# Performance work log

Hardware: AMD Instinct MI355X
Metric: run time of the kernel (lower is better)

## Reference

```python
import jax, jax.numpy as jnp
import numpy as np

B, S = 128, 400
EMB, ENC, DEC = 128, 1024, 300
VOCAB, MAX_OOV = 50000, 50


def setup_inputs() -> dict:
    key = jax.random.key(0)
    ks = jax.random.split(key, 16)
    s = 0.05
    return {
        "embedded": jax.random.normal(ks[0], (B, EMB), jnp.float32),
        "enc_output": jax.random.normal(ks[1], (B, S, ENC), jnp.float32),
        "h1": jax.random.normal(ks[2], (B, DEC), jnp.float32),
        "pad_mask": jnp.zeros((B, S), jnp.bool_),
        "max_n_oov": MAX_OOV,
        "source_WORD_encoding_extended": jax.random.randint(ks[3], (B, S), 0, VOCAB + MAX_OOV),
        # parameters
        "W_attn1": jax.random.normal(ks[4], (ENC, DEC), jnp.float32) * s,
        "W_attn2": jax.random.normal(ks[5], (ENC, DEC), jnp.float32) * s,
        "W_ih": jax.random.normal(ks[6], (3 * DEC, EMB + ENC), jnp.float32) * s,
        "W_hh": jax.random.normal(ks[7], (3 * DEC, DEC), jnp.float32) * s,
        "b_ih": jax.random.normal(ks[8], (3 * DEC,), jnp.float32) * s,
        "b_hh": jax.random.normal(ks[9], (3 * DEC,), jnp.float32) * s,
        "W_out": jax.random.normal(ks[10], (VOCAB, ENC + DEC), jnp.float32) * s,
        "b_out": jax.random.normal(ks[11], (VOCAB,), jnp.float32) * s,
        "W_p": jax.random.normal(ks[12], (1, ENC + DEC), jnp.float32) * s,
        "b_p": jax.random.normal(ks[13], (1,), jnp.float32) * s,
    }


def _additive_attn(h, enc_output, W, pad_mask):
    # h: [B, DEC], enc_output: [B, S, ENC], W: [ENC, DEC]
    e = jnp.einsum('bse,ed->bsd', enc_output, W)
    scores = jnp.einsum('bd,bsd->bs', h, e)
    scores = jnp.where(pad_mask, -jnp.inf, scores)
    return jax.nn.softmax(scores, axis=1)  # [B, S]


def _gru_cell(x, h, W_ih, W_hh, b_ih, b_hh):
    gx = x @ W_ih.T + b_ih  # [B, 3*DEC]
    gh = h @ W_hh.T + b_hh
    xr, xz, xn = jnp.split(gx, 3, axis=1)
    hr, hz, hn = jnp.split(gh, 3, axis=1)
    r = jax.nn.sigmoid(xr + hr)
    z = jax.nn.sigmoid(xz + hz)
    n = jnp.tanh(xn + r * hn)
    return (1.0 - z) * n + z * h


def reference(embedded, enc_output, h1, pad_mask, max_n_oov,
              source_WORD_encoding_extended, W_attn1, W_attn2,
              W_ih, W_hh, b_ih, b_hh, W_out, b_out, W_p, b_p):
    a = _additive_attn(h1, enc_output, W_attn1, pad_mask)
    weighted = jnp.einsum('bs,bse->be', a, enc_output)
    rnn_input = jnp.concatenate([embedded, weighted], axis=1)
    h_new = _gru_cell(rnn_input, h1, W_ih, W_hh, b_ih, b_hh)

    a2 = _additive_attn(h_new, enc_output, W_attn2, pad_mask)
    weighted2 = jnp.einsum('bs,bse->be', a2, enc_output)
    hw = jnp.concatenate([h_new, weighted2], axis=1)  # [B, DEC+ENC]

    p_vocab = jax.nn.softmax(hw @ W_out.T + b_out, axis=1)  # [B, VOCAB]
    p_gen = jax.nn.sigmoid(hw @ W_p.T + b_p)  # [B, 1]

    bsz = p_vocab.shape[0]
    ext_zeros = jnp.zeros((bsz, max_n_oov), p_vocab.dtype)
    p_out = p_gen * jnp.concatenate([p_vocab, ext_zeros], axis=1)
    rows = jnp.arange(bsz)[:, None]
    p_out = p_out.at[rows, source_WORD_encoding_extended].add((1.0 - p_gen) * a2)
    return p_out, h_new
```

## Files before the change

### kernel.cpp

```cpp
#include <hip/hip_runtime.h>
#include <stdint.h>

constexpr int B_     = 128;
constexpr int S_     = 400;
constexpr int EMB_   = 128;
constexpr int ENC_   = 1024;
constexpr int DEC_   = 300;
constexpr int VOCAB_ = 50000;
constexpr int OOV_   = 50;
constexpr int OUTW_  = VOCAB_ + OOV_;
constexpr int KHW_   = ENC_ + DEC_;
constexpr int KHWP_  = 1344;
constexpr int G3_    = 3 * DEC_;
constexpr int KIN_   = EMB_ + ENC_;
constexpr int CHK_   = 64;
constexpr int CHKB_  = 128;
constexpr int NC_    = 21;
constexpr int PSTRIDE_ = 1028;
constexpr int NTILE_ = 782;
constexpr int NSPL_  = 6;
constexpr int ROWS_  = 67;
constexpr int NBLK_  = 768;

typedef __attribute__((ext_vector_type(4))) float f32x4;
typedef __attribute__((ext_vector_type(8))) short short8;

__device__ __forceinline__ float dot4(float4 a, float4 b) {
  return a.x * b.x + a.y * b.y + a.z * b.z + a.w * b.w;
}

__device__ __forceinline__ short f2bf(float f) {
  uint32_t u = __builtin_bit_cast(uint32_t, f);
  u += 0x7fffu + ((u >> 16) & 1u);
  return (short)(u >> 16);
}

__device__ __forceinline__ void gbar(int* bar, int target) {
  __syncthreads();
  if (threadIdx.x == 0) {
    __hip_atomic_fetch_add(bar, 1, __ATOMIC_RELEASE, __HIP_MEMORY_SCOPE_AGENT);
    while (__hip_atomic_load(bar, __ATOMIC_ACQUIRE, __HIP_MEMORY_SCOPE_AGENT) < target)
      __builtin_amdgcn_s_sleep(8);
  }
  __syncthreads();
}


__device__ void ph_compute_v(const float* __restrict__ W, const float* __restrict__ h,
                             float* __restrict__ v, int b, int tid, float* hs) {
  for (int d = tid; d < DEC_; d += 256) hs[d] = h[b * DEC_ + d];
  __syncthreads();
  for (int e = tid; e < ENC_; e += 256) {
    const float4* w4 = (const float4*)(W + (size_t)e * DEC_);
    const float4* h4 = (const float4*)hs;
    float acc = 0.f;
    #pragma unroll 5
    for (int d = 0; d < DEC_ / 4; ++d) acc += dot4(w4[d], h4[d]);
    v[b * ENC_ + e] = acc;
  }
  __syncthreads();
}

__device__ void ph_attn(const float* __restrict__ enc, const float* __restrict__ v,
                        float* __restrict__ scores, float* __restrict__ part,
                        int b, int split, int tid) {
  int wave = tid >> 6, lane = tid & 63;
  float4 vr[4];
  #pragma unroll
  for (int c = 0; c < 4; ++c) vr[c] = *(const float4*)(v + b * ENC_ + c * 256 + lane * 4);
  float m = -INFINITY, l = 0.f;
  float4 wa[4];
  #pragma unroll
  for (int c = 0; c < 4; ++c) wa[c] = make_float4(0.f, 0.f, 0.f, 0.f);
  int s0 = split * ROWS_;
  int s_end = min(s0 + ROWS_, S_);
  int s = s0 + wave;
  for (; s + 4 < s_end; s += 8) {
    const float* era = enc + ((size_t)b * S_ + s) * ENC_;
    const float* erb = enc + ((size_t)b * S_ + s + 4) * ENC_;
    float4 e4a[4], e4b[4];
    #pragma unroll
    for (int c = 0; c < 4; ++c) {
      e4a[c] = *(const float4*)(era + c * 256 + lane * 4);
      e4b[c] = *(const float4*)(erb + c * 256 + lane * 4);
    }
    float pa = 0.f, pb = 0.f;
    #pragma unroll
    for (int c = 0; c < 4; ++c) { pa += dot4(e4a[c], vr[c]); pb += dot4(e4b[c], vr[c]); }
    #pragma unroll
    for (int off = 32; off; off >>= 1) {
      pa += __shfl_xor(pa, off);
      pb += __shfl_xor(pb, off);
    }
    if (lane == 0) { scores[b * S_ + s] = pa; scores[b * S_ + s + 4] = pb; }
    float nm = fmaxf(m, fmaxf(pa, pb));
    float sc = __expf(m - nm);
    float ea = __expf(pa - nm);
    float eb = __expf(pb - nm);
    l = l * sc + ea + eb;
    #pragma unroll
    for (int c = 0; c < 4; ++c) {
      wa[c].x = wa[c].x * sc + ea * e4a[c].x + eb * e4b[c].x;
      wa[c].y = wa[c].y * sc + ea * e4a[c].y + eb * e4b[c].y;
      wa[c].z = wa[c].z * sc + ea * e4a[c].z + eb * e4b[c].z;
      wa[c].w = wa[c].w * sc + ea * e4a[c].w + eb * e4b[c].w;
    }
    m = nm;
  }
  if (s < s_end) {
    const float* er = enc + ((size_t)b * S_ + s) * ENC_;
    float4 e4[4];
    #pragma unroll
    for (int c = 0; c < 4; ++c) e4[c] = *(const float4*)(er + c * 256 + lane * 4);
    float p = 0.f;
    #pragma unroll
    for (int c = 0; c < 4; ++c) p += dot4(e4[c], vr[c]);
    #pragma unroll
    for (int off = 32; off; off >>= 1) p += __shfl_xor(p, off);
    if (lane == 0) scores[b * S_ + s] = p;
    float nm = fmaxf(m, p);
    float sc = __expf(m - nm), pe = __expf(p - nm);
    l = l * sc + pe;
    #pragma unroll
    for (int c = 0; c < 4; ++c) {
      wa[c].x = wa[c].x * sc + pe * e4[c].x;
      wa[c].y = wa[c].y * sc + pe * e4[c].y;
      wa[c].z = wa[c].z * sc + pe * e4[c].z;
      wa[c].w = wa[c].w * sc + pe * e4[c].w;
    }
    m = nm;
  }
  float* pp = part + ((size_t)b * (NSPL_ * 4) + split * 4 + wave) * PSTRIDE_;
  #pragma unroll
  for (int c = 0; c < 4; ++c) *(float4*)(pp + c * 256 + lane * 4) = wa[c];
  if (lane == 0) { pp[1024] = m; pp[1025] = l; }
}

__device__ void ph_merge1(const float* __restrict__ part, float* __restrict__ wout,
                          int b, int tid, float* smemf) {
  constexpr int P = NSPL_ * 4;
  const float* pb = part + (size_t)b * P * PSTRIDE_;
  float* scl = smemf;
  float* Lsp = smemf + 64;
  if (tid < 64) {
    float mp = (tid < P) ? pb[tid * PSTRIDE_ + 1024] : -INFINITY;
    float lp = (tid < P) ? pb[tid * PSTRIDE_ + 1025] : 0.f;
    float M = mp;
    #pragma unroll
    for (int off = 32; off; off >>= 1) M = fmaxf(M, __shfl_xor(M, off));
    float e = (lp > 0.f) ? __expf(mp - M) : 0.f;
    scl[tid] = e;
    float Lc = lp * e;
    #pragma unroll
    for (int off = 32; off; off >>= 1) Lc += __shfl_xor(Lc, off);
    if (tid == 0) Lsp[0] = Lc;
  }
  __syncthreads();
  float invL = 1.f / Lsp[0];
  for (int e = tid; e < ENC_; e += 256) {
    float acc = 0.f;
    for (int p = 0; p < P; ++p) acc += scl[p] * pb[p * PSTRIDE_ + e];
    wout[(size_t)b * ENC_ + e] = acc * invL;
  }
  __syncthreads();
}

__device__ void ph_merge2(const float* __restrict__ part, short* __restrict__ hwb,
                          float* __restrict__ ml, const float* __restrict__ W_p,
                          const float* __restrict__ b_p, const float* __restrict__ pg_acc,
                          float* __restrict__ pg, int b, int tid, float* smemf) {
  constexpr int P = NSPL_ * 4;
  const float* pb = part + (size_t)b * P * PSTRIDE_;
  float* scl = smemf;
  float* Lsp = smemf + 64;
  float* red = smemf + 80;
  if (tid < 64) {
    float mp = (tid < P) ? pb[tid * PSTRIDE_ + 1024] : -INFINITY;
    float lp = (tid < P) ? pb[tid * PSTRIDE_ + 1025] : 0.f;
    float M = mp;
    #pragma unroll
    for (int off = 32; off; off >>= 1) M = fmaxf(M, __shfl_xor(M, off));
    float e = (lp > 0.f) ? __expf(mp - M) : 0.f;
    scl[tid] = e;
    float Lc = lp * e;
    #pragma unroll
    for (int off = 32; off; off >>= 1) Lc += __shfl_xor(Lc, off);
    if (tid == 0) { Lsp[0] = Lc; ml[b * 2] = M; ml[b * 2 + 1] = Lc; }
  }
  __syncthreads();
  float invL = 1.f / Lsp[0];
  float pacc = 0.f;
  for (int e = tid; e < ENC_; e += 256) {
    float acc = 0.f;
    for (int p = 0; p < P; ++p) acc += scl[p] * pb[p * PSTRIDE_ + e];
    float w = acc * invL;
    hwb[(size_t)b * KHWP_ + DEC_ + e] = f2bf(w);
    pacc += w * W_p[DEC_ + e];
  }
  if (tid < KHWP_ - KHW_) hwb[(size_t)b * KHWP_ + KHW_ + tid] = 0;
  red[tid] = pacc;
  __syncthreads();
  for (int st = 128; st > 0; st >>= 1) {
    if (tid < st) red[tid] += red[tid + st];
    __syncthreads();
  }
  if (tid == 0) pg[b] = 1.f / (1.f + __expf(-(red[0] + pg_acc[b] + b_p[0])));
  __syncthreads();
}

__device__ void ph_gates(const float* __restrict__ emb, const float* __restrict__ wgt,
                         const float* __restrict__ h1, const float* __restrict__ W_ih,
                         const float* __restrict__ W_hh, const float* __restrict__ b_ih,
                         const float* __restrict__ b_hh, float* __restrict__ gx,
                         float* __restrict__ gh, float* __restrict__ pg_acc,
                         int bid, int nblk, int tid) {
  int idx0 = bid * 256 + tid;
  if (idx0 < B_) pg_acc[idx0] = 0.f;
  for (int idx = idx0; idx < G3_ * B_; idx += nblk * 256) {
    int b = idx & (B_ - 1);
    int g = idx >> 7;
    const float4* wr = (const float4*)(W_ih + (size_t)g * KIN_);
    const float4* xe = (const float4*)(emb + b * EMB_);
    const float4* xw = (const float4*)(wgt + b * ENC_);
    float accx = b_ih[g];
    #pragma unroll 8
    for (int k = 0; k < EMB_ / 4; ++k) accx += dot4(wr[k], xe[k]);
    #pragma unroll 8
    for (int k = 0; k < ENC_ / 4; ++k) accx += dot4(wr[EMB_ / 4 + k], xw[k]);
    const float4* wh = (const float4*)(W_hh + (size_t)g * DEC_);
    const float4* xh = (const float4*)(h1 + b * DEC_);
    float acch = b_hh[g];
    #pragma unroll 5
    for (int k = 0; k < DEC_ / 4; ++k) acch += dot4(wh[k], xh[k]);
    gx[g * B_ + b] = accx;
    gh[g * B_ + b] = acch;
  }
}

__device__ void ph_gru(const float* __restrict__ gx, const float* __restrict__ gh,
                       const float* __restrict__ h1, float* __restrict__ hn,
                       short* __restrict__ hwb, float* __restrict__ outh,
                       const float* __restrict__ W_p, float* __restrict__ pg_acc,
                       int b, int j0, int tid, float* red) {
  int j = j0 + tid;
  float pp = 0.f;
  if (j < DEC_) {
    float xr = gx[j * B_ + b], xz = gx[(j + DEC_) * B_ + b], xn = gx[(j + 2 * DEC_) * B_ + b];
    float hr = gh[j * B_ + b], hz = gh[(j + DEC_) * B_ + b], hnn = gh[(j + 2 * DEC_) * B_ + b];
    float r = 1.f / (1.f + __expf(-(xr + hr)));
    float z = 1.f / (1.f + __expf(-(xz + hz)));
    float n = tanhf(xn + r * hnn);
    float h = (1.f - z) * n + z * h1[b * DEC_ + j];
    hn[b * DEC_ + j] = h;
    hwb[(size_t)b * KHWP_ + j] = f2bf(h);
    outh[b * DEC_ + j] = h;
    pp = h * W_p[j];
  }
  red[tid] = pp;
  __syncthreads();
  for (int st = 128; st > 0; st >>= 1) {
    if (tid < st) red[tid] += red[tid + st];
    __syncthreads();
  }
  if (tid == 0) atomicAdd(pg_acc + b, red[0]);
  __syncthreads();
}

__device__ void ph_outproj(int tile, int tid, const short* __restrict__ A,
                           const float* __restrict__ Wo, const float* __restrict__ bo,
                           float* __restrict__ out, float* __restrict__ pml, char* smem) {
  short* A_lds = (short*)smem;
  int wave = tid >> 6, lane = tid & 63;
  int r16 = lane & 15, kg = lane >> 4;
  int vcol = tile * 64 + wave * 16 + r16;
  int vload = vcol < VOCAB_ ? vcol : VOCAB_ - 1;
  const float* brow = Wo + (size_t)vload * KHW_ + kg * 8;
  f32x4 acc[8];
  #pragma unroll
  for (int mi = 0; mi < 8; ++mi) acc[mi] = (f32x4){0.f, 0.f, 0.f, 0.f};

  const char* A8 = (const char*)A;
  uint32_t srcoff[4];
  #pragma unroll
  for (int i = 0; i < 4; ++i) {
    int g = tid + i * 256;
    int row = g >> 3, sp = g & 7;
    int sl = sp ^ (row & 7);
    srcoff[i] = (uint32_t)(row * 2688 + sl * 16);
  }

  float4 br[2][4];
  float  tl[8];

  #pragma unroll
  for (int i = 0; i < 4; ++i)
    __builtin_amdgcn_global_load_lds(
        (const __attribute__((address_space(1))) void*)(A8 + srcoff[i]),
        (__attribute__((address_space(3))) void*)((char*)A_lds + i * 4096 + wave * 1024),
        16, 0, 0);
  #pragma unroll
  for (int s = 0; s < 2; ++s) {
    br[0][2 * s]     = *(const float4*)(brow + s * 32);
    br[0][2 * s + 1] = *(const float4*)(brow + s * 32 + 4);
  }

  #pragma unroll
  for (int c = 0; c < NC_; ++c) {
    __syncthreads();
    if (c < NC_ - 1) {
      char* dstb = (char*)A_lds + ((c + 1) & 1) * 16384;
      #pragma unroll
      for (int i = 0; i < 4; ++i)
        __builtin_amdgcn_global_load_lds(
            (const __attribute__((address_space(1))) void*)(A8 + srcoff[i] + (c + 1) * CHKB_),
            (__attribute__((address_space(3))) void*)(dstb + i * 4096 + wave * 1024),
            16, 0, 0);
      if (c + 1 < NC_ - 1) {
        #pragma unroll
        for (int s = 0; s < 2; ++s) {
          br[(c + 1) & 1][2 * s]     = *(const float4*)(brow + (c + 1) * CHK_ + s * 32);
          br[(c + 1) & 1][2 * s + 1] = *(const float4*)(brow + (c + 1) * CHK_ + s * 32 + 4);
        }
      } else {
        br[0][0] = *(const float4*)(brow + 20 * CHK_);
        br[0][1] = *(const float4*)(brow + 20 * CHK_ + 4);
        #pragma unroll
        for (int j = 0; j < 8; ++j)
          tl[j] = (kg * 8 + j < KHW_ - 1312) ? brow[1312 + j] : 0.f;
      }
    }
    const char* rbase = (const char*)A_lds + (c & 1) * 16384 + r16 * CHKB_;
    #pragma unroll
    for (int s = 0; s < 2; ++s) {
      short8 bf;
      if (c == NC_ - 1 && s == 1) {
        #pragma unroll
        for (int j = 0; j < 8; ++j) bf[j] = f2bf(tl[j]);
      } else {
        float4 b0 = br[c & 1][2 * s], b1 = br[c & 1][2 * s + 1];
        bf[0] = f2bf(b0.x); bf[1] = f2bf(b0.y); bf[2] = f2bf(b0.z); bf[3] = f2bf(b0.w);
        bf[4] = f2bf(b1.x); bf[5] = f2bf(b1.y); bf[6] = f2bf(b1.z); bf[7] = f2bf(b1.w);
      }
      int sl = ((s << 2) + kg) ^ (r16 & 7);
      #pragma unroll
      for (int mi = 0; mi < 8; ++mi) {
        short8 af = *(const short8*)(rbase + mi * 2048 + (sl << 4));
        acc[mi] = __builtin_amdgcn_mfma_f32_16x16x32_bf16(af, bf, acc[mi], 0, 0, 0);
      }
    }
  }

  __syncthreads();
  float* wml = (float*)A_lds;

  bool valid = vcol < VOCAB_;
  float biasv = bo[vload];
  #pragma unroll
  for (int mi = 0; mi < 8; ++mi) {
    #pragma unroll
    for (int j = 0; j < 4; ++j) {
      float lv = valid ? acc[mi][j] + biasv : -INFINITY;
      if (valid) out[(size_t)(mi * 16 + kg * 4 + j) * OUTW_ + vcol] = lv;
      float mr = lv;
      #pragma unroll
      for (int msk = 1; msk < 16; msk <<= 1) mr = fmaxf(mr, __shfl_xor(mr, msk));
      float se = valid ? __expf(lv - mr) : 0.f;
      #pragma unroll
      for (int msk = 1; msk < 16; msk <<= 1) se += __shfl_xor(se, msk);
      if (r16 == 0) {
        wml[(wave * B_ + mi * 16 + kg * 4 + j) * 2]     = mr;
        wml[(wave * B_ + mi * 16 + kg * 4 + j) * 2 + 1] = se;
      }
    }
  }
  __syncthreads();
  if (tid < B_) {
    float M = -INFINITY;
    #pragma unroll
    for (int w = 0; w < 4; ++w) M = fmaxf(M, wml[(w * B_ + tid) * 2]);
    float L = 0.f;
    #pragma unroll
    for (int w = 0; w < 4; ++w) {
      float lw = wml[(w * B_ + tid) * 2 + 1];
      if (lw > 0.f) L += lw * __expf(wml[(w * B_ + tid) * 2] - M);
    }
    pml[((size_t)tile * B_ + tid) * 2]     = M;
    pml[((size_t)tile * B_ + tid) * 2 + 1] = L;
  }
}

__device__ void ph_vfinal(int bq, int b, int tid, float* __restrict__ out,
                          const float* __restrict__ pml, const float* __restrict__ pg,
                          const int* __restrict__ src, const float* __restrict__ scores,
                          const float* __restrict__ ml2, float* smemf) {
  float* rm = smemf;
  float* rl = smemf + 256;
  float lm = -INFINITY, ll = 0.f;
  for (int tile = tid; tile < NTILE_; tile += 256) {
    float m = pml[((size_t)tile * B_ + b) * 2];
    float l = pml[((size_t)tile * B_ + b) * 2 + 1];
    float M = fmaxf(lm, m);
    float nl = 0.f;
    if (ll > 0.f) nl += ll * __expf(lm - M);
    if (l > 0.f) nl += l * __expf(m - M);
    lm = M; ll = nl;
  }
  rm[tid] = lm; rl[tid] = ll;
  __syncthreads();
  for (int st = 128; st > 0; st >>= 1) {
    if (tid < st) {
      float m1 = rm[tid], l1 = rl[tid], m2 = rm[tid + st], l2 = rl[tid + st];
      float M = fmaxf(m1, m2);
      float L = (l1 > 0.f ? l1 * __expf(m1 - M) : 0.f) + (l2 > 0.f ? l2 * __expf(m2 - M) : 0.f);
      rm[tid] = M; rl[tid] = L;
    }
    __syncthreads();
  }
  float M = rm[0], L = rl[0];
  float p = pg[b];
  float scale = p / L;
  float* row = out + (size_t)b * OUTW_;
  int lo = bq * 12513;
  int hi = min(lo + 12513, OUTW_);
  for (int v = lo + tid; v < hi; v += 256)
    row[v] = (v < VOCAB_) ? scale * __expf(row[v] - M) : 0.f;
  __syncthreads();
  float M2 = ml2[b * 2], L2 = ml2[b * 2 + 1];
  float q = (1.f - p) / L2;
  for (int s = tid; s < S_; s += 256) {
    int cidx = src[b * S_ + s];
    if (cidx >= lo && cidx < hi)
      atomicAdd(row + cidx, q * __expf(scores[b * S_ + s] - M2));
  }
}


__global__ __launch_bounds__(256) void k_mega1(
    const float* embedded, const float* enc, const float* h1,
    const float* W1, const float* W2, const float* W_ih, const float* W_hh,
    const float* b_ih, const float* b_hh, const float* W_p, const float* b_p,
    float* out, float* v_ws, float* w1_ws, float* gx_ws, float* gh_ws, float* hn_ws,
    float* sc_ws, float* ml2_ws, float* pg_ws, float* pga_ws,
    short* hwb_ws, float* part_ws, int* bar) {
  __shared__ __align__(16) float smem[512];
  int bid = blockIdx.x, tid = threadIdx.x;
  if (bid < B_) ph_compute_v(W1, h1, v_ws, bid, tid, smem);
  gbar(bar, 1 * NBLK_);
  ph_attn(enc, v_ws, sc_ws, part_ws, bid / NSPL_, bid % NSPL_, tid);
  gbar(bar, 2 * NBLK_);
  if (bid < B_) ph_merge1(part_ws, w1_ws, bid, tid, smem);
  gbar(bar, 3 * NBLK_);
  ph_gates(embedded, w1_ws, h1, W_ih, W_hh, b_ih, b_hh, gx_ws, gh_ws, pga_ws, bid, NBLK_, tid);
  gbar(bar, 4 * NBLK_);
  if (bid < 2 * B_)
    ph_gru(gx_ws, gh_ws, h1, hn_ws, hwb_ws, out + (size_t)B_ * OUTW_, W_p, pga_ws,
           bid >> 1, (bid & 1) * 256, tid, smem);
  gbar(bar, 5 * NBLK_);
  if (bid < B_) ph_compute_v(W2, hn_ws, v_ws, bid, tid, smem);
  gbar(bar, 6 * NBLK_);
  ph_attn(enc, v_ws, sc_ws, part_ws, bid / NSPL_, bid % NSPL_, tid);
  gbar(bar, 7 * NBLK_);
  if (bid < B_) ph_merge2(part_ws, hwb_ws, ml2_ws, W_p, b_p, pga_ws, pg_ws, bid, tid, smem);
}


__global__ __launch_bounds__(256) void k_compute_v(const float* W, const float* h, float* v) {
  __shared__ __align__(16) float hs[DEC_];
  ph_compute_v(W, h, v, blockIdx.x, threadIdx.x, hs);
}
__global__ __launch_bounds__(256) void k_attn_pass(const float* enc, const float* v,
                                                   float* scores, float* part) {
  ph_attn(enc, v, scores, part, blockIdx.x, blockIdx.y, threadIdx.x);
}
__global__ __launch_bounds__(256) void k_attn_merge1(const float* part, float* wout) {
  __shared__ __align__(16) float sm[80];
  ph_merge1(part, wout, blockIdx.x, threadIdx.x, sm);
}
__global__ __launch_bounds__(256) void k_attn_merge2(const float* part, short* hwb, float* ml,
                                                     const float* W_p, const float* b_p,
                                                     const float* pga, float* pg) {
  __shared__ __align__(16) float sm[336];
  ph_merge2(part, hwb, ml, W_p, b_p, pga, pg, blockIdx.x, threadIdx.x, sm);
}
__global__ __launch_bounds__(256) void k_gates(const float* emb, const float* wgt,
                                               const float* h1, const float* W_ih,
                                               const float* W_hh, const float* b_ih,
                                               const float* b_hh, float* gx, float* gh,
                                               float* pga) {
  ph_gates(emb, wgt, h1, W_ih, W_hh, b_ih, b_hh, gx, gh, pga, blockIdx.x, gridDim.x,
           threadIdx.x);
}
__global__ __launch_bounds__(256) void k_gru_combine(const float* gx, const float* gh,
                                                     const float* h1, float* hn, short* hwb,
                                                     float* outh, const float* W_p,
                                                     float* pga) {
  __shared__ __align__(16) float red[256];
  ph_gru(gx, gh, h1, hn, hwb, outh, W_p, pga, blockIdx.y, blockIdx.x * 256, threadIdx.x, red);
}
__global__ __launch_bounds__(256) void k_outproj(const short* A, const float* Wo,
                                                 const float* bo, float* out, float* pml) {
  __shared__ __align__(16) char smem[2 * B_ * CHK_ * 2];
  ph_outproj(blockIdx.x, threadIdx.x, A, Wo, bo, out, pml, smem);
}
__global__ __launch_bounds__(256) void k_vfinal(float* out, const float* pml, const float* pg,
                                                const int* src, const float* scores,
                                                const float* ml2) {
  __shared__ __align__(16) float sm[512];
  ph_vfinal(blockIdx.x, blockIdx.y, threadIdx.x, out, pml, pg, src, scores, ml2, sm);
}

extern "C" void kernel_launch(void* const* d_in, const int* in_sizes, int n_in,
                              void* d_out, int out_size, void* d_ws, size_t ws_size,
                              hipStream_t stream) {
  const float* embedded = (const float*)d_in[0];
  const float* enc      = (const float*)d_in[1];
  const float* h1       = (const float*)d_in[2];
  const int*   src      = (const int*)d_in[5];
  const float* W1       = (const float*)d_in[6];
  const float* W2       = (const float*)d_in[7];
  const float* W_ih     = (const float*)d_in[8];
  const float* W_hh     = (const float*)d_in[9];
  const float* b_ih     = (const float*)d_in[10];
  const float* b_hh     = (const float*)d_in[11];
  const float* W_out    = (const float*)d_in[12];
  const float* b_out    = (const float*)d_in[13];
  const float* W_p      = (const float*)d_in[14];
  const float* b_p      = (const float*)d_in[15];
  float* out = (float*)d_out;
  float* ws  = (float*)d_ws;

  size_t off = 0;
  float* v_ws    = ws + off; off += (size_t)B_ * ENC_;
  float* w1_ws   = ws + off; off += (size_t)B_ * ENC_;
  float* gx_ws   = ws + off; off += (size_t)G3_ * B_;
  float* gh_ws   = ws + off; off += (size_t)G3_ * B_;
  float* hn_ws   = ws + off; off += (size_t)B_ * DEC_;
  float* sc_ws   = ws + off; off += (size_t)B_ * S_;
  float* ml2_ws  = ws + off; off += 256;
  float* pg_ws   = ws + off; off += 128;
  float* pga_ws  = ws + off; off += 128;
  int*   bar_ws  = (int*)(ws + off); off += 64;
  float* pml_ws  = ws + off; off += (size_t)NTILE_ * B_ * 2;
  short* hwb_ws  = (short*)(ws + off); off += (size_t)B_ * KHWP_ / 2;
  float* part_ws = ws + off;

  hipMemsetAsync(bar_ws, 0, 256, stream);

  int occ = 0;
  hipOccupancyMaxActiveBlocksPerMultiprocessor(&occ, (const void*)k_mega1, 256, 0);

  if (occ >= 3) {
    k_mega1<<<NBLK_, 256, 0, stream>>>(
        embedded, enc, h1, W1, W2, W_ih, W_hh, b_ih, b_hh, W_p, b_p, out,
        v_ws, w1_ws, gx_ws, gh_ws, hn_ws, sc_ws, ml2_ws, pg_ws, pga_ws,
        hwb_ws, part_ws, bar_ws);
  } else {
    k_compute_v<<<B_, 256, 0, stream>>>(W1, h1, v_ws);
    k_attn_pass<<<dim3(B_, NSPL_), 256, 0, stream>>>(enc, v_ws, sc_ws, part_ws);
    k_attn_merge1<<<B_, 256, 0, stream>>>(part_ws, w1_ws);
    k_gates<<<(G3_ * B_) / 256, 256, 0, stream>>>(embedded, w1_ws, h1, W_ih, W_hh, b_ih,
                                                  b_hh, gx_ws, gh_ws, pga_ws);
    k_gru_combine<<<dim3(2, B_), 256, 0, stream>>>(gx_ws, gh_ws, h1, hn_ws, hwb_ws,
                                                   out + (size_t)B_ * OUTW_, W_p, pga_ws);
    k_compute_v<<<B_, 256, 0, stream>>>(W2, hn_ws, v_ws);
    k_attn_pass<<<dim3(B_, NSPL_), 256, 0, stream>>>(enc, v_ws, sc_ws, part_ws);
    k_attn_merge2<<<B_, 256, 0, stream>>>(part_ws, hwb_ws, ml2_ws, W_p, b_p, pga_ws, pg_ws);
  }
  k_outproj<<<NTILE_, 256, 0, stream>>>(hwb_ws, W_out, b_out, out, pml_ws);
  k_vfinal<<<dim3(4, B_), 256, 0, stream>>>(out, pml_ws, pg_ws, src, sc_ws, ml2_ws);
}
```

Measured before the change: 429.2 us.

## Fuse attention merge, GRU gates, GRU update and second v-projection per batch row

```diff
diff --git a/kernel.cpp b/kernel.cpp
--- a/kernel.cpp
+++ b/kernel.cpp
@@ -40,7 +40,7 @@
   if (threadIdx.x == 0) {
     __hip_atomic_fetch_add(bar, 1, __ATOMIC_RELEASE, __HIP_MEMORY_SCOPE_AGENT);
     while (__hip_atomic_load(bar, __ATOMIC_ACQUIRE, __HIP_MEMORY_SCOPE_AGENT) < target)
-      __builtin_amdgcn_s_sleep(8);
+      __builtin_amdgcn_s_sleep(32);
   }
   __syncthreads();
 }
@@ -205,6 +205,93 @@
     __syncthreads();
   }
   if (tid == 0) pg[b] = 1.f / (1.f + __expf(-(red[0] + pg_acc[b] + b_p[0])));
+  __syncthreads();
+}
+
+__device__ void ph_fused_mid(const float* __restrict__ part, const float* __restrict__ emb,
+                             const float* __restrict__ h1, const float* __restrict__ W_ih,
+                             const float* __restrict__ W_hh, const float* __restrict__ b_ih,
+                             const float* __restrict__ b_hh, const float* __restrict__ W2,
+                             const float* __restrict__ W_p, float* __restrict__ v_ws,
+                             short* __restrict__ hwb, float* __restrict__ outh,
+                             float* __restrict__ pga, int b, int tid, float* sm) {
+  constexpr int P = NSPL_ * 4;
+  float* w1  = sm;
+  float* scl = sm + 1024;
+  float* Lsp = sm + 1088;
+  float* hsh = sm + 1104;
+  float* gxs = sm + 1408;
+  float* ghs = sm + 2308;
+  float* red = sm + 3208;
+  const float* pb = part + (size_t)b * P * PSTRIDE_;
+  if (tid < 64) {
+    float mp = (tid < P) ? pb[tid * PSTRIDE_ + 1024] : -INFINITY;
+    float lp = (tid < P) ? pb[tid * PSTRIDE_ + 1025] : 0.f;
+    float M = mp;
+    #pragma unroll
+    for (int off = 32; off; off >>= 1) M = fmaxf(M, __shfl_xor(M, off));
+    float e = (lp > 0.f) ? __expf(mp - M) : 0.f;
+    scl[tid] = e;
+    float Lc = lp * e;
+    #pragma unroll
+    for (int off = 32; off; off >>= 1) Lc += __shfl_xor(Lc, off);
+    if (tid == 0) Lsp[0] = Lc;
+  }
+  __syncthreads();
+  float invL = 1.f / Lsp[0];
+  for (int e = tid; e < ENC_; e += 256) {
+    float acc = 0.f;
+    for (int p = 0; p < P; ++p) acc += scl[p] * pb[p * PSTRIDE_ + e];
+    w1[e] = acc * invL;
+  }
+  __syncthreads();
+  for (int g = tid; g < G3_; g += 256) {
+    const float4* wr = (const float4*)(W_ih + (size_t)g * KIN_);
+    const float4* xe = (const float4*)(emb + b * EMB_);
+    const float4* xw = (const float4*)w1;
+    float accx = b_ih[g];
+    #pragma unroll 8
+    for (int k = 0; k < EMB_ / 4; ++k) accx += dot4(wr[k], xe[k]);
+    #pragma unroll 8
+    for (int k = 0; k < ENC_ / 4; ++k) accx += dot4(wr[EMB_ / 4 + k], xw[k]);
+    const float4* wh = (const float4*)(W_hh + (size_t)g * DEC_);
+    const float4* xh = (const float4*)(h1 + b * DEC_);
+    float acch = b_hh[g];
+    #pragma unroll 5
+    for (int k = 0; k < DEC_ / 4; ++k) acch += dot4(wh[k], xh[k]);
+    gxs[g] = accx;
+    ghs[g] = acch;
+  }
+  __syncthreads();
+  for (int j = tid; j < DEC_; j += 256) {
+    float xr = gxs[j], xz = gxs[j + DEC_], xn = gxs[j + 2 * DEC_];
+    float hr = ghs[j], hz = ghs[j + DEC_], hnn = ghs[j + 2 * DEC_];
+    float r = 1.f / (1.f + __expf(-(xr + hr)));
+    float z = 1.f / (1.f + __expf(-(xz + hz)));
+    float n = tanhf(xn + r * hnn);
+    float h = (1.f - z) * n + z * h1[b * DEC_ + j];
+    hsh[j] = h;
+    hwb[(size_t)b * KHWP_ + j] = f2bf(h);
+    outh[b * DEC_ + j] = h;
+  }
+  __syncthreads();
+  float pp = 0.f;
+  for (int j = tid; j < DEC_; j += 256) pp += hsh[j] * W_p[j];
+  red[tid] = pp;
+  __syncthreads();
+  for (int st = 128; st > 0; st >>= 1) {
+    if (tid < st) red[tid] += red[tid + st];
+    __syncthreads();
+  }
+  if (tid == 0) pga[b] = red[0];
+  for (int e = tid; e < ENC_; e += 256) {
+    const float4* w4 = (const float4*)(W2 + (size_t)e * DEC_);
+    const float4* h4 = (const float4*)hsh;
+    float acc = 0.f;
+    #pragma unroll 5
+    for (int d = 0; d < DEC_ / 4; ++d) acc += dot4(w4[d], h4[d]);
+    v_ws[b * ENC_ + e] = acc;
+  }
   __syncthreads();
 }
 
@@ -435,31 +522,24 @@
 }
 
 
-__global__ __launch_bounds__(256) void k_mega1(
+__global__ __launch_bounds__(256) void k_mega2(
     const float* embedded, const float* enc, const float* h1,
     const float* W1, const float* W2, const float* W_ih, const float* W_hh,
     const float* b_ih, const float* b_hh, const float* W_p, const float* b_p,
-    float* out, float* v_ws, float* w1_ws, float* gx_ws, float* gh_ws, float* hn_ws,
-    float* sc_ws, float* ml2_ws, float* pg_ws, float* pga_ws,
+    float* out, float* v_ws, float* sc_ws, float* ml2_ws, float* pg_ws, float* pga_ws,
     short* hwb_ws, float* part_ws, int* bar) {
-  __shared__ __align__(16) float smem[512];
+  __shared__ __align__(16) float smem[3584];
   int bid = blockIdx.x, tid = threadIdx.x;
   if (bid < B_) ph_compute_v(W1, h1, v_ws, bid, tid, smem);
   gbar(bar, 1 * NBLK_);
   ph_attn(enc, v_ws, sc_ws, part_ws, bid / NSPL_, bid % NSPL_, tid);
   gbar(bar, 2 * NBLK_);
-  if (bid < B_) ph_merge1(part_ws, w1_ws, bid, tid, smem);
+  if (bid < B_)
+    ph_fused_mid(part_ws, embedded, h1, W_ih, W_hh, b_ih, b_hh, W2, W_p,
+                 v_ws, hwb_ws, out + (size_t)B_ * OUTW_, pga_ws, bid, tid, smem);
   gbar(bar, 3 * NBLK_);
-  ph_gates(embedded, w1_ws, h1, W_ih, W_hh, b_ih, b_hh, gx_ws, gh_ws, pga_ws, bid, NBLK_, tid);
+  ph_attn(enc, v_ws, sc_ws, part_ws, bid / NSPL_, bid % NSPL_, tid);
   gbar(bar, 4 * NBLK_);
-  if (bid < 2 * B_)
-    ph_gru(gx_ws, gh_ws, h1, hn_ws, hwb_ws, out + (size_t)B_ * OUTW_, W_p, pga_ws,
-           bid >> 1, (bid & 1) * 256, tid, smem);
-  gbar(bar, 5 * NBLK_);
-  if (bid < B_) ph_compute_v(W2, hn_ws, v_ws, bid, tid, smem);
-  gbar(bar, 6 * NBLK_);
-  ph_attn(enc, v_ws, sc_ws, part_ws, bid / NSPL_, bid % NSPL_, tid);
-  gbar(bar, 7 * NBLK_);
   if (bid < B_) ph_merge2(part_ws, hwb_ws, ml2_ws, W_p, b_p, pga_ws, pg_ws, bid, tid, smem);
 }
 
@@ -547,13 +627,12 @@
   hipMemsetAsync(bar_ws, 0, 256, stream);
 
   int occ = 0;
-  hipOccupancyMaxActiveBlocksPerMultiprocessor(&occ, (const void*)k_mega1, 256, 0);
+  hipOccupancyMaxActiveBlocksPerMultiprocessor(&occ, (const void*)k_mega2, 256, 0);
 
   if (occ >= 3) {
-    k_mega1<<<NBLK_, 256, 0, stream>>>(
+    k_mega2<<<NBLK_, 256, 0, stream>>>(
         embedded, enc, h1, W1, W2, W_ih, W_hh, b_ih, b_hh, W_p, b_p, out,
-        v_ws, w1_ws, gx_ws, gh_ws, hn_ws, sc_ws, ml2_ws, pg_ws, pga_ws,
-        hwb_ws, part_ws, bar_ws);
+        v_ws, sc_ws, ml2_ws, pg_ws, pga_ws, hwb_ws, part_ws, bar_ws);
   } else {
     k_compute_v<<<B_, 256, 0, stream>>>(W1, h1, v_ws);
     k_attn_pass<<<dim3(B_, NSPL_), 256, 0, stream>>>(enc, v_ws, sc_ws, part_ws);
```

Result: no change. 427.4 us (median of 2 runs) (-0.4%).
